# Kernel optimization log

Measured on AMD Instinct MI355X. Metric: run time of the kernel, lower is better.

The kernel has to match this reference:

```python
import jax, jax.numpy as jnp
import numpy as np
from jax.scipy.linalg import expm


def setup_inputs() -> dict:
    key = jax.random.key(0)
    k1, k2, k3 = jax.random.split(key, 3)
    B, T, d = 64, 4096, 16
    Z = jax.random.normal(k1, (B, T, 2), dtype=jnp.float32)
    A1 = jax.random.normal(k2, (d, d), dtype=jnp.float32)
    A2 = jax.random.normal(k3, (d, d), dtype=jnp.float32)
    return {"Z": Z, "A1": A1, "A2": A2}


def reference(Z, A1, A2):
    # Z: [B, T, 2]; A1, A2: [d, d] learned params
    d = A1.shape[0]
    S1 = A1 - A1.T  # skew-symmetric
    S2 = A2 - A2.T
    # per-timestep increment matrices: expm(z1*S1 + z2*S2), shape [B, T, d, d]
    G = Z[..., 0, None, None] * S1 + Z[..., 1, None, None] * S2
    M = expm(G)
    # X_0 = I; X_t = X_{t-1} @ M[:, t] for t = 1..T-1  (M[:, 0] is unused,
    # exactly as in the original loop starting at t=1).
    matmul = lambda a, b: jnp.einsum('...ij,...jk->...ik', a, b)
    prefix = jax.lax.associative_scan(matmul, M[:, 1:], axis=1)  # [B, T-1, d, d]
    eye = jnp.broadcast_to(jnp.eye(d, dtype=Z.dtype), (Z.shape[0], 1, d, d))
    A = jnp.concatenate([eye, prefix], axis=1)  # [B, T, d, d]
    B_inv = jnp.linalg.inv(A)
    return (A, B_inv)
```

## Files before the change

### kernel.cpp

```cpp
#include <hip/hip_runtime.h>

#define NB 64
#define NT 4096
#define CH 8
#define KC (NT/CH)
#define GPB 16
#define NA 128
#define NM 14
#define PI_F 3.14159265358979f

#define C3c (1.f/6.f)
#define C4c (1.f/24.f)
#define C5c (1.f/120.f)
#define C6c (1.f/720.f)
#define C7c (1.f/5040.f)
#define C8c (1.f/40320.f)

template<int K>
__device__ __forceinline__ void mm_step(float acc[16], const float a[16], const float b[16]) {
  float bb[16];
#pragma unroll
  for (int e = 0; e < 16; ++e)
    bb[e] = __int_as_float(__builtin_amdgcn_ds_swizzle(__float_as_int(b[e]), (K << 7) | 0x13));
#pragma unroll
  for (int rr = 0; rr < 4; ++rr) {
    const float a0 = __int_as_float(__builtin_amdgcn_mov_dpp(__float_as_int(a[rr*4+0]), K*0x55, 0xF, 0xF, true));
    const float a1 = __int_as_float(__builtin_amdgcn_mov_dpp(__float_as_int(a[rr*4+1]), K*0x55, 0xF, 0xF, true));
    const float a2 = __int_as_float(__builtin_amdgcn_mov_dpp(__float_as_int(a[rr*4+2]), K*0x55, 0xF, 0xF, true));
    const float a3 = __int_as_float(__builtin_amdgcn_mov_dpp(__float_as_int(a[rr*4+3]), K*0x55, 0xF, 0xF, true));
#pragma unroll
    for (int cc = 0; cc < 4; ++cc)
      acc[rr*4+cc] = fmaf(a3, bb[12+cc], fmaf(a2, bb[8+cc], fmaf(a1, bb[4+cc], fmaf(a0, bb[cc], acc[rr*4+cc]))));
  }
}
__device__ __forceinline__ void mmreg(float acc[16], const float a[16], const float b[16]) {
  mm_step<0>(acc, a, b); mm_step<1>(acc, a, b);
  mm_step<2>(acc, a, b); mm_step<3>(acc, a, b);
}

__global__ __launch_bounds__(256) void k0_prep(const float* __restrict__ A1,
                                               const float* __restrict__ A2,
                                               float* __restrict__ ws) {
  __shared__ float S[2][256], W2[4][256], W3[8][256], W4[16][256];
  const int tid = threadIdx.x;
  {
    int i_ = tid >> 4, j_ = tid & 15;
    S[0][tid] = A1[i_*16+j_] - A1[j_*16+i_];
    S[1][tid] = A2[i_*16+j_] - A2[j_*16+i_];
  }
  __syncthreads();
  const int i = tid >> 4, j = tid & 15;
#pragma unroll
  for (int p = 0; p < 4; ++p) {
    const float* a = S[p>>1]; const float* bm = S[p&1];
    float acc = 0.f;
    for (int k = 0; k < 16; ++k) acc = fmaf(a[i*16+k], bm[k*16+j], acc);
    W2[p][tid] = acc;
  }
  __syncthreads();
#pragma unroll
  for (int p = 0; p < 8; ++p) {
    const float* a = S[p>>2]; const float* bm = W2[p&3];
    float acc = 0.f;
    for (int k = 0; k < 16; ++k) acc = fmaf(a[i*16+k], bm[k*16+j], acc);
    W3[p][tid] = acc;
  }
  __syncthreads();
#pragma unroll
  for (int p = 0; p < 16; ++p) {
    const float* a = S[p>>3]; const float* bm = W3[p&7];
    float acc = 0.f;
    for (int k = 0; k < 16; ++k) acc = fmaf(a[i*16+k], bm[k*16+j], acc);
    W4[p][tid] = acc;
  }
  __syncthreads();
  float* M = ws + NA;
  M[ 0*256+tid] = S[0][tid];
  M[ 1*256+tid] = S[1][tid];
  M[ 2*256+tid] = W2[0][tid];
  M[ 3*256+tid] = W2[1][tid] + W2[2][tid];
  M[ 4*256+tid] = W2[3][tid];
  M[ 5*256+tid] = W3[0][tid];
  M[ 6*256+tid] = W3[1][tid] + W3[2][tid] + W3[4][tid];
  M[ 7*256+tid] = W3[3][tid] + W3[5][tid] + W3[6][tid];
  M[ 8*256+tid] = W3[7][tid];
  M[ 9*256+tid] = W4[0][tid];
  M[10*256+tid] = W4[1][tid] + W4[2][tid] + W4[4][tid] + W4[8][tid];
  M[11*256+tid] = W4[3][tid] + W4[5][tid] + W4[6][tid] + W4[9][tid] + W4[10][tid] + W4[12][tid];
  M[12*256+tid] = W4[7][tid] + W4[11][tid] + W4[13][tid] + W4[14][tid];
  M[13*256+tid] = W4[15][tid];
  if (tid < NA) {
    const float th = (float)tid * (PI_F / NA);
    const float c = cosf(th), s = sinf(th);
    float v[16];
    float n2 = 0.f;
#pragma unroll
    for (int jj = 0; jj < 16; ++jj) { v[jj] = sinf(1.7f*(float)(jj+1) + th) + 0.25f; n2 += v[jj]*v[jj]; }
    float inv = rsqrtf(n2);
#pragma unroll
    for (int jj = 0; jj < 16; ++jj) v[jj] *= inv;
    float lam = 0.f;
    for (int it = 0; it < 14; ++it) {
      float w[16];
#pragma unroll
      for (int ii = 0; ii < 16; ++ii) {
        float a1 = 0.f, a2 = 0.f;
#pragma unroll
        for (int jj = 0; jj < 16; ++jj) { a1 = fmaf(S[0][ii*16+jj], v[jj], a1); a2 = fmaf(S[1][ii*16+jj], v[jj], a2); }
        w[ii] = c*a1 + s*a2;
      }
      n2 = 0.f;
#pragma unroll
      for (int ii = 0; ii < 16; ++ii) n2 += w[ii]*w[ii];
      lam = sqrtf(n2);
      inv = (lam > 1e-20f) ? 1.f/lam : 0.f;
#pragma unroll
      for (int ii = 0; ii < 16; ++ii) v[ii] = w[ii]*inv;
    }
    ws[tid] = lam * 1.05f;
  }
}

__global__ __launch_bounds__(256, 2) void k1_chunk(const float* __restrict__ Z,
                                                   const float* __restrict__ wsrc,
                                                   float* __restrict__ Aout)
{
  __shared__ float Qs[NM*256];
  __shared__ float rhos[NA];
  const int tid = threadIdx.x;
  for (int e = tid; e < NM*256; e += 256) Qs[e] = wsrc[NA + e];
  if (tid < NA) rhos[tid] = wsrc[tid];
  __syncthreads();

  const int g  = tid >> 4;
  const int u  = tid & 15;
  const int tr = u >> 2;
  const int tc = u & 3;
  const int gw = (tid & 63) >> 4;
  const int qbase = (4*tr)*16 + 4*tc;

  const int cid    = blockIdx.x * GPB + g;
  const int b      = cid >> 9;
  const int kchunk = cid & (KC-1);
  const int t0     = kchunk * CH;

  const float trtc = (tr == tc) ? 1.f : 0.f;
  const int tz = t0 + u;
  float2 za = *(const float2*)&Z[(size_t)(b*NT + (tz < NT ? tz : NT-1)) * 2];

  float lt[16];
#pragma unroll
  for (int rr = 0; rr < 4; ++rr)
#pragma unroll
    for (int cc = 0; cc < 4; ++cc) lt[rr*4+cc] = (rr == cc) ? trtc : 0.f;

  const int fstep = (kchunk == 0) ? 1 : 0;

  for (int tt = 0; tt < CH; ++tt) {
    const size_t obase = (size_t)(b*NT + t0 + tt) * 256 + (size_t)(tr*64) + 4*tc;

    const int src = (gw << 4) + tt;
    float z1 = __shfl(za.x, src);
    float z2 = __shfl(za.y, src);
    float r_ = sqrtf(z1*z1 + z2*z2);
    float th = atan2f(z2, z1);
    if (th < 0.f) th += PI_F;
    int idx = ((int)(th * ((float)NA / PI_F) + 0.5f)) & (NA - 1);
    float nrm = r_ * rhos[idx];
    nrm = fmaxf(nrm, __shfl_xor(nrm, 16));
    nrm = fmaxf(nrm, __shfl_xor(nrm, 32));
    int s = 0;
    if (nrm > 1.0f) s = (int)ceilf(log2f(nrm));
    const float scl = exp2f(-(float)s);

    if (kchunk == 0 && tt == 0) {
#pragma unroll
      for (int rr = 0; rr < 4; ++rr)
        *(float4*)&Aout[obase + rr*16] =
          make_float4(lt[rr*4+0], lt[rr*4+1], lt[rr*4+2], lt[rr*4+3]);
      continue;
    }

    const float x = z1*scl, y = z2*scl;
    const float x2 = x*x, xy = x*y, y2 = y*y;
    const float x3 = x2*x, x2y = x2*y, xy2 = x*y2, y3 = y2*y;
    const float zc[NM] = { x, y, x2, xy, y2, x3, x2y, xy2, y3,
                           x2*x2, x3*y, x2*y2, x*y3, y2*y2 };
    const float WP[NM] = { 1.f,1.f, .5f,.5f,.5f, C3c,C3c,C3c,C3c, 0.f,0.f,0.f,0.f,0.f };
    const float WU[NM] = { C5c,C5c, C6c,C6c,C6c, C7c,C7c,C7c,C7c, C8c,C8c,C8c,C8c,C8c };

    float pp[16], uu[16], g4[16];
#pragma unroll
    for (int rr = 0; rr < 4; ++rr)
#pragma unroll
      for (int cc = 0; cc < 4; ++cc) {
        pp[rr*4+cc] = (rr == cc) ? trtc : 0.f;
        uu[rr*4+cc] = (rr == cc) ? trtc * C4c : 0.f;
        g4[rr*4+cc] = 0.f;
      }
#pragma unroll
    for (int m = 0; m < NM; ++m) {
      const float am = zc[m] * WP[m];
      const float bm = zc[m] * WU[m];
#pragma unroll
      for (int rr = 0; rr < 4; ++rr) {
        float4 v = *(const float4*)&Qs[m*256 + rr*16 + qbase];
        if (m < 9) {
          pp[rr*4+0] = fmaf(am, v.x, pp[rr*4+0]);
          pp[rr*4+1] = fmaf(am, v.y, pp[rr*4+1]);
          pp[rr*4+2] = fmaf(am, v.z, pp[rr*4+2]);
          pp[rr*4+3] = fmaf(am, v.w, pp[rr*4+3]);
        } else {
          g4[rr*4+0] = fmaf(zc[m], v.x, g4[rr*4+0]);
          g4[rr*4+1] = fmaf(zc[m], v.y, g4[rr*4+1]);
          g4[rr*4+2] = fmaf(zc[m], v.z, g4[rr*4+2]);
          g4[rr*4+3] = fmaf(zc[m], v.w, g4[rr*4+3]);
        }
        uu[rr*4+0] = fmaf(bm, v.x, uu[rr*4+0]);
        uu[rr*4+1] = fmaf(bm, v.y, uu[rr*4+1]);
        uu[rr*4+2] = fmaf(bm, v.z, uu[rr*4+2]);
        uu[rr*4+3] = fmaf(bm, v.w, uu[rr*4+3]);
      }
    }

    mmreg(pp, g4, uu);

    for (int q = 0; q < s; ++q) {
      float acc[16];
#pragma unroll
      for (int e = 0; e < 16; ++e) acc[e] = 0.f;
      mmreg(acc, pp, pp);
#pragma unroll
      for (int e = 0; e < 16; ++e) pp[e] = acc[e];
    }
    if (tt == fstep) {
#pragma unroll
      for (int e = 0; e < 16; ++e) lt[e] = pp[e];
    } else {
      float acc[16];
#pragma unroll
      for (int e = 0; e < 16; ++e) acc[e] = 0.f;
      mmreg(acc, lt, pp);
#pragma unroll
      for (int e = 0; e < 16; ++e) lt[e] = acc[e];
    }
#pragma unroll
    for (int rr = 0; rr < 4; ++rr)
      *(float4*)&Aout[obase + rr*16] =
        make_float4(lt[rr*4+0], lt[rr*4+1], lt[rr*4+2], lt[rr*4+3]);
  }
}

#define ROWB 72
#define MATS (4*ROWB)
#define LGS (2*MATS + 8)
#define BX 0
#define BY MATS
#define WSYNC() asm volatile("s_waitcnt lgkmcnt(0)" ::: "memory")

#define MM_FMA(A_, B0_, B1_, B2_, B3_, base) \
  acc[base+0] = fmaf(A_.w, B3_.x, fmaf(A_.z, B2_.x, fmaf(A_.y, B1_.x, fmaf(A_.x, B0_.x, acc[base+0])))); \
  acc[base+1] = fmaf(A_.w, B3_.y, fmaf(A_.z, B2_.y, fmaf(A_.y, B1_.y, fmaf(A_.x, B0_.y, acc[base+1])))); \
  acc[base+2] = fmaf(A_.w, B3_.z, fmaf(A_.z, B2_.z, fmaf(A_.y, B1_.z, fmaf(A_.x, B0_.z, acc[base+2])))); \
  acc[base+3] = fmaf(A_.w, B3_.w, fmaf(A_.z, B2_.w, fmaf(A_.y, B1_.w, fmaf(A_.x, B0_.w, acc[base+3]))));

template<bool CLR>
__device__ __forceinline__ void mmg(float acc[16], const float* sb, int offA, int offB,
                                    const int xA[4], const int xB[4], int trR) {
  if (CLR) {
#pragma unroll
    for (int e = 0; e < 16; ++e) acc[e] = 0.f;
  }
#pragma unroll
  for (int kk = 0; kk < 4; ++kk) {
    const float* pa = sb + offA + trR + xA[kk];
    const float* pb = sb + offB + kk*ROWB + xB[kk];
    float4 a0 = *(const float4*)(pa +  0);
    float4 a1 = *(const float4*)(pa + 16);
    float4 a2 = *(const float4*)(pa + 32);
    float4 a3 = *(const float4*)(pa + 48);
    float4 b0 = *(const float4*)(pb +  0);
    float4 b1 = *(const float4*)(pb + 16);
    float4 b2 = *(const float4*)(pb + 32);
    float4 b3 = *(const float4*)(pb + 48);
    MM_FMA(a0, b0, b1, b2, b3, 0)
    MM_FMA(a1, b0, b1, b2, b3, 4)
    MM_FMA(a2, b0, b1, b2, b3, 8)
    MM_FMA(a3, b0, b1, b2, b3, 12)
  }
}

__device__ __forceinline__ void st4(float* sb, int offD, const float v[16], int trR, int xD) {
  float* p = sb + offD + trR + xD;
#pragma unroll
  for (int rr = 0; rr < 4; ++rr)
    *(float4*)(p + rr*16) = make_float4(v[rr*4+0], v[rr*4+1], v[rr*4+2], v[rr*4+3]);
}

__global__ __launch_bounds__(256) void k2a(const float* __restrict__ Aout,
                                           float* __restrict__ Binv) {
  __shared__ float Cy[256], Lt[256];
  const int tid = threadIdx.x, i = tid >> 4, j = tid & 15;
  const int b = blockIdx.x >> 5, sb = blockIdx.x & 31;
  Cy[tid] = (i == j) ? 1.f : 0.f;
  float nxt = Aout[((size_t)(b*NT + (sb*16)*CH + CH - 1))*256 + tid];
  __syncthreads();
  for (int q = 0; q < 16; ++q) {
    const int k = sb*16 + q;
    Binv[((size_t)(b*NT + k*CH))*256 + tid] = Cy[tid];
    Lt[tid] = nxt;
    __syncthreads();
    if (q < 15) nxt = Aout[((size_t)(b*NT + (k+1)*CH + CH - 1))*256 + tid];
    float a2 = 0.f;
#pragma unroll
    for (int m = 0; m < 16; ++m) a2 = fmaf(Cy[i*16+m], Lt[m*16+j], a2);
    __syncthreads();
    Cy[tid] = a2;
    __syncthreads();
  }
  Binv[((size_t)(b*NT + sb*128 + 1))*256 + tid] = Cy[tid];
}

__global__ __launch_bounds__(256) void k2b(float* __restrict__ Binv) {
  __shared__ float Cy[256], Lt[256];
  const int tid = threadIdx.x, i = tid >> 4, j = tid & 15;
  const int b = blockIdx.x;
  Cy[tid] = (i == j) ? 1.f : 0.f;
  float nxt = Binv[((size_t)(b*NT + 1))*256 + tid];
  __syncthreads();
  for (int sb2 = 0; sb2 < 32; ++sb2) {
    Binv[((size_t)(b*NT + sb2*128 + 2))*256 + tid] = Cy[tid];
    Lt[tid] = nxt;
    __syncthreads();
    if (sb2 < 31) nxt = Binv[((size_t)(b*NT + (sb2+1)*128 + 1))*256 + tid];
    float a2 = 0.f;
#pragma unroll
    for (int m = 0; m < 16; ++m) a2 = fmaf(Cy[i*16+m], Lt[m*16+j], a2);
    __syncthreads();
    Cy[tid] = a2;
    __syncthreads();
  }
}

__global__ __launch_bounds__(256, 2) void k3_apply(float* __restrict__ Aout,
                                                   float* __restrict__ Binv)
{
  __shared__ __align__(16) float lds[GPB * LGS];
  __shared__ float SupL[256];
  const int tid = threadIdx.x;
  const int g   = tid >> 4;
  const int u   = tid & 15;
  const int tr  = u >> 2;
  const int tc  = u & 3;
  const int trR = tr * ROWB;
  float* sb_ = lds + g * LGS;
  const int xA[4] = { ((0^tr)<<2), ((1^tr)<<2), ((2^tr)<<2), ((3^tr)<<2) };
  const int xB[4] = { ((tc^0)<<2), ((tc^1)<<2), ((tc^2)<<2), ((tc^3)<<2) };
  const int xD    = ((tc^tr)<<2);

  const int b   = blockIdx.x >> 5;
  const int sbq = blockIdx.x & 31;
  const int k   = sbq*16 + g;
  const int t0  = k * CH;

  SupL[tid] = Binv[((size_t)(b*NT + sbq*128 + 2))*256 + tid];
  {
    const float* srcp = &Binv[((size_t)(b*NT + k*CH))*256];
#pragma unroll
    for (int rr = 0; rr < 4; ++rr) {
      float4 v = *(const float4*)&srcp[rr*64 + 4*u];
      *(float4*)&sb_[BX + rr*ROWB + tr*16 + ((tc^rr)<<2)] = v;
    }
  }
  __syncthreads();

  float wt[16];
  {
    float* acc = wt;
#pragma unroll
    for (int e = 0; e < 16; ++e) acc[e] = 0.f;
#pragma unroll
    for (int kk = 0; kk < 4; ++kk) {
      const float* pb = sb_ + BX + kk*ROWB + xB[kk];
      float4 b0 = *(const float4*)(pb +  0);
      float4 b1 = *(const float4*)(pb + 16);
      float4 b2 = *(const float4*)(pb + 32);
      float4 b3 = *(const float4*)(pb + 48);
      float4 a0 = *(const float4*)&SupL[(4*tr+0)*16 + 4*kk];
      float4 a1 = *(const float4*)&SupL[(4*tr+1)*16 + 4*kk];
      float4 a2 = *(const float4*)&SupL[(4*tr+2)*16 + 4*kk];
      float4 a3 = *(const float4*)&SupL[(4*tr+3)*16 + 4*kk];
      MM_FMA(a0, b0, b1, b2, b3, 0)
      MM_FMA(a1, b0, b1, b2, b3, 4)
      MM_FMA(a2, b0, b1, b2, b3, 8)
      MM_FMA(a3, b0, b1, b2, b3, 12)
    }
  }
  st4(sb_, BY, wt, trR, xD);
  WSYNC();

  float acc[16];
  for (int tt = 0; tt < CH; ++tt) {
    const size_t base = ((size_t)(b*NT + t0 + tt))*256;
#pragma unroll
    for (int rr = 0; rr < 4; ++rr) {
      float4 v = *(const float4*)&Aout[base + rr*64 + 4*u];
      *(float4*)&sb_[BX + rr*ROWB + tr*16 + ((tc^rr)<<2)] = v;
    }
    WSYNC();
    mmg<true>(acc, sb_, BY, BX, xA, xB, trR);
    const size_t obase = base + (size_t)(tr*64) + 4*tc;
#pragma unroll
    for (int rr = 0; rr < 4; ++rr)
      *(float4*)&Aout[obase + rr*16] =
        make_float4(acc[rr*4+0], acc[rr*4+1], acc[rr*4+2], acc[rr*4+3]);
    st4(sb_, BX, acc, trR, xD); WSYNC();
    const float* pt = sb_ + BX + tc*ROWB + ((tr^tc)<<2);
    float4 f0 = *(const float4*)(pt +  0);
    float4 f1 = *(const float4*)(pt + 16);
    float4 f2 = *(const float4*)(pt + 32);
    float4 f3 = *(const float4*)(pt + 48);
    *(float4*)&Binv[obase +  0] = make_float4(f0.x, f1.x, f2.x, f3.x);
    *(float4*)&Binv[obase + 16] = make_float4(f0.y, f1.y, f2.y, f3.y);
    *(float4*)&Binv[obase + 32] = make_float4(f0.z, f1.z, f2.z, f3.z);
    *(float4*)&Binv[obase + 48] = make_float4(f0.w, f1.w, f2.w, f3.w);
    WSYNC();
  }
}

extern "C" void kernel_launch(void* const* d_in, const int* in_sizes, int n_in,
                              void* d_out, int out_size, void* d_ws, size_t ws_size,
                              hipStream_t stream) {
  const float* Z  = (const float*)d_in[0];
  const float* A1 = (const float*)d_in[1];
  const float* A2 = (const float*)d_in[2];
  float* ws   = (float*)d_ws;
  float* Aout = (float*)d_out;
  float* Binv = Aout + (size_t)NB * NT * 256;

  k0_prep<<<1, 256, 0, stream>>>(A1, A2, ws);
  k1_chunk<<<NB * KC / GPB, 256, 0, stream>>>(Z, ws, Aout);
  k2a<<<NB * 32, 256, 0, stream>>>(Aout, Binv);
  k2b<<<NB, 256, 0, stream>>>(Binv);
  k3_apply<<<NB * 32, 256, 0, stream>>>(Aout, Binv);
}
```

Measured before the change: 542.5 us.

## Replace serial carry scans with parallel Hillis-Steele scans and register-tiled apply

```diff
diff --git a/kernel.cpp b/kernel.cpp
--- a/kernel.cpp
+++ b/kernel.cpp
@@ -8,6 +8,7 @@
 #define NA 128
 #define NM 14
 #define PI_F 3.14159265358979f
+#define XPAD 20
 
 #define C3c (1.f/6.f)
 #define C4c (1.f/24.f)
@@ -36,6 +37,20 @@
 __device__ __forceinline__ void mmreg(float acc[16], const float a[16], const float b[16]) {
   mm_step<0>(acc, a, b); mm_step<1>(acc, a, b);
   mm_step<2>(acc, a, b); mm_step<3>(acc, a, b);
+}
+
+__device__ __forceinline__ void ld_tile(float p[16], const float* base, int tr, int tc) {
+#pragma unroll
+  for (int rr = 0; rr < 4; ++rr) {
+    float4 v = *(const float4*)&base[(4*tr+rr)*16 + 4*tc];
+    p[rr*4+0]=v.x; p[rr*4+1]=v.y; p[rr*4+2]=v.z; p[rr*4+3]=v.w;
+  }
+}
+__device__ __forceinline__ void st_tile(float* base, const float p[16], int tr, int tc) {
+#pragma unroll
+  for (int rr = 0; rr < 4; ++rr)
+    *(float4*)&base[(4*tr+rr)*16 + 4*tc] =
+      make_float4(p[rr*4+0], p[rr*4+1], p[rr*4+2], p[rr*4+3]);
 }
 
 __global__ __launch_bounds__(256) void k0_prep(const float* __restrict__ A1,
@@ -251,180 +266,142 @@
   }
 }
 
-#define ROWB 72
-#define MATS (4*ROWB)
-#define LGS (2*MATS + 8)
-#define BX 0
-#define BY MATS
-#define WSYNC() asm volatile("s_waitcnt lgkmcnt(0)" ::: "memory")
-
-#define MM_FMA(A_, B0_, B1_, B2_, B3_, base) \
-  acc[base+0] = fmaf(A_.w, B3_.x, fmaf(A_.z, B2_.x, fmaf(A_.y, B1_.x, fmaf(A_.x, B0_.x, acc[base+0])))); \
-  acc[base+1] = fmaf(A_.w, B3_.y, fmaf(A_.z, B2_.y, fmaf(A_.y, B1_.y, fmaf(A_.x, B0_.y, acc[base+1])))); \
-  acc[base+2] = fmaf(A_.w, B3_.z, fmaf(A_.z, B2_.z, fmaf(A_.y, B1_.z, fmaf(A_.x, B0_.z, acc[base+2])))); \
-  acc[base+3] = fmaf(A_.w, B3_.w, fmaf(A_.z, B2_.w, fmaf(A_.y, B1_.w, fmaf(A_.x, B0_.w, acc[base+3]))));
-
-template<bool CLR>
-__device__ __forceinline__ void mmg(float acc[16], const float* sb, int offA, int offB,
-                                    const int xA[4], const int xB[4], int trR) {
-  if (CLR) {
-#pragma unroll
-    for (int e = 0; e < 16; ++e) acc[e] = 0.f;
-  }
-#pragma unroll
-  for (int kk = 0; kk < 4; ++kk) {
-    const float* pa = sb + offA + trR + xA[kk];
-    const float* pb = sb + offB + kk*ROWB + xB[kk];
-    float4 a0 = *(const float4*)(pa +  0);
-    float4 a1 = *(const float4*)(pa + 16);
-    float4 a2 = *(const float4*)(pa + 32);
-    float4 a3 = *(const float4*)(pa + 48);
-    float4 b0 = *(const float4*)(pb +  0);
-    float4 b1 = *(const float4*)(pb + 16);
-    float4 b2 = *(const float4*)(pb + 32);
-    float4 b3 = *(const float4*)(pb + 48);
-    MM_FMA(a0, b0, b1, b2, b3, 0)
-    MM_FMA(a1, b0, b1, b2, b3, 4)
-    MM_FMA(a2, b0, b1, b2, b3, 8)
-    MM_FMA(a3, b0, b1, b2, b3, 12)
-  }
-}
-
-__device__ __forceinline__ void st4(float* sb, int offD, const float v[16], int trR, int xD) {
-  float* p = sb + offD + trR + xD;
-#pragma unroll
-  for (int rr = 0; rr < 4; ++rr)
-    *(float4*)(p + rr*16) = make_float4(v[rr*4+0], v[rr*4+1], v[rr*4+2], v[rr*4+3]);
-}
 
 __global__ __launch_bounds__(256) void k2a(const float* __restrict__ Aout,
                                            float* __restrict__ Binv) {
-  __shared__ float Cy[256], Lt[256];
-  const int tid = threadIdx.x, i = tid >> 4, j = tid & 15;
+  __shared__ float xch[16*16*XPAD];
+  const int tid = threadIdx.x;
+  const int g = tid >> 4, u = tid & 15, tr = u >> 2, tc = u & 3;
   const int b = blockIdx.x >> 5, sb = blockIdx.x & 31;
-  Cy[tid] = (i == j) ? 1.f : 0.f;
-  float nxt = Aout[((size_t)(b*NT + (sb*16)*CH + CH - 1))*256 + tid];
-  __syncthreads();
-  for (int q = 0; q < 16; ++q) {
-    const int k = sb*16 + q;
-    Binv[((size_t)(b*NT + k*CH))*256 + tid] = Cy[tid];
-    Lt[tid] = nxt;
+  const int k = sb*16 + g;
+
+  float p[16];
+  ld_tile(p, &Aout[((size_t)(b*NT + k*CH + CH-1))*256], tr, tc);
+
+#pragma unroll
+  for (int r = 1; r < 16; r <<= 1) {
+    float* mine = &xch[(g*16+u)*XPAD];
+#pragma unroll
+    for (int rr = 0; rr < 4; ++rr)
+      *(float4*)&mine[4*rr] = make_float4(p[rr*4+0], p[rr*4+1], p[rr*4+2], p[rr*4+3]);
     __syncthreads();
-    if (q < 15) nxt = Aout[((size_t)(b*NT + (k+1)*CH + CH - 1))*256 + tid];
-    float a2 = 0.f;
-#pragma unroll
-    for (int m = 0; m < 16; ++m) a2 = fmaf(Cy[i*16+m], Lt[m*16+j], a2);
+    if (g >= r) {
+      const float* nb = &xch[((g-r)*16+u)*XPAD];
+      float a[16];
+#pragma unroll
+      for (int rr = 0; rr < 4; ++rr) {
+        float4 v = *(const float4*)&nb[4*rr];
+        a[rr*4+0]=v.x; a[rr*4+1]=v.y; a[rr*4+2]=v.z; a[rr*4+3]=v.w;
+      }
+      float acc[16];
+#pragma unroll
+      for (int e = 0; e < 16; ++e) acc[e] = 0.f;
+      mmreg(acc, a, p);
+#pragma unroll
+      for (int e = 0; e < 16; ++e) p[e] = acc[e];
+    }
     __syncthreads();
-    Cy[tid] = a2;
+  }
+
+  const float trtc = (tr == tc) ? 1.f : 0.f;
+  if (g == 0) {
+    float idt[16];
+#pragma unroll
+    for (int rr = 0; rr < 4; ++rr)
+#pragma unroll
+      for (int cc = 0; cc < 4; ++cc) idt[rr*4+cc] = (rr == cc) ? trtc : 0.f;
+    st_tile(&Binv[((size_t)(b*NT + k*CH))*256], idt, tr, tc);
+  }
+  if (g < 15)
+    st_tile(&Binv[((size_t)(b*NT + (k+1)*CH))*256], p, tr, tc);
+  else
+    st_tile(&Binv[((size_t)(b*NT + 128*sb + 1))*256], p, tr, tc);
+}
+
+__global__ __launch_bounds__(512) void k2b(float* __restrict__ Binv) {
+  __shared__ float xch[32*16*XPAD];
+  const int tid = threadIdx.x;
+  const int g = tid >> 4, u = tid & 15, tr = u >> 2, tc = u & 3;
+  const int b = blockIdx.x;
+
+  float p[16];
+  ld_tile(p, &Binv[((size_t)(b*NT + 128*g + 1))*256], tr, tc);
+
+#pragma unroll
+  for (int r = 1; r < 32; r <<= 1) {
+    float* mine = &xch[(g*16+u)*XPAD];
+#pragma unroll
+    for (int rr = 0; rr < 4; ++rr)
+      *(float4*)&mine[4*rr] = make_float4(p[rr*4+0], p[rr*4+1], p[rr*4+2], p[rr*4+3]);
     __syncthreads();
-  }
-  Binv[((size_t)(b*NT + sb*128 + 1))*256 + tid] = Cy[tid];
-}
-
-__global__ __launch_bounds__(256) void k2b(float* __restrict__ Binv) {
-  __shared__ float Cy[256], Lt[256];
-  const int tid = threadIdx.x, i = tid >> 4, j = tid & 15;
-  const int b = blockIdx.x;
-  Cy[tid] = (i == j) ? 1.f : 0.f;
-  float nxt = Binv[((size_t)(b*NT + 1))*256 + tid];
-  __syncthreads();
-  for (int sb2 = 0; sb2 < 32; ++sb2) {
-    Binv[((size_t)(b*NT + sb2*128 + 2))*256 + tid] = Cy[tid];
-    Lt[tid] = nxt;
+    if (g >= r) {
+      const float* nb = &xch[((g-r)*16+u)*XPAD];
+      float a[16];
+#pragma unroll
+      for (int rr = 0; rr < 4; ++rr) {
+        float4 v = *(const float4*)&nb[4*rr];
+        a[rr*4+0]=v.x; a[rr*4+1]=v.y; a[rr*4+2]=v.z; a[rr*4+3]=v.w;
+      }
+      float acc[16];
+#pragma unroll
+      for (int e = 0; e < 16; ++e) acc[e] = 0.f;
+      mmreg(acc, a, p);
+#pragma unroll
+      for (int e = 0; e < 16; ++e) p[e] = acc[e];
+    }
     __syncthreads();
-    if (sb2 < 31) nxt = Binv[((size_t)(b*NT + (sb2+1)*128 + 1))*256 + tid];
-    float a2 = 0.f;
-#pragma unroll
-    for (int m = 0; m < 16; ++m) a2 = fmaf(Cy[i*16+m], Lt[m*16+j], a2);
-    __syncthreads();
-    Cy[tid] = a2;
-    __syncthreads();
-  }
+  }
+
+  const float trtc = (tr == tc) ? 1.f : 0.f;
+  if (g == 0) {
+    float idt[16];
+#pragma unroll
+    for (int rr = 0; rr < 4; ++rr)
+#pragma unroll
+      for (int cc = 0; cc < 4; ++cc) idt[rr*4+cc] = (rr == cc) ? trtc : 0.f;
+    st_tile(&Binv[((size_t)(b*NT + 2))*256], idt, tr, tc);
+  }
+  if (g < 31)
+    st_tile(&Binv[((size_t)(b*NT + 128*(g+1) + 2))*256], p, tr, tc);
 }
 
 __global__ __launch_bounds__(256, 2) void k3_apply(float* __restrict__ Aout,
                                                    float* __restrict__ Binv)
 {
-  __shared__ __align__(16) float lds[GPB * LGS];
-  __shared__ float SupL[256];
   const int tid = threadIdx.x;
-  const int g   = tid >> 4;
-  const int u   = tid & 15;
-  const int tr  = u >> 2;
-  const int tc  = u & 3;
-  const int trR = tr * ROWB;
-  float* sb_ = lds + g * LGS;
-  const int xA[4] = { ((0^tr)<<2), ((1^tr)<<2), ((2^tr)<<2), ((3^tr)<<2) };
-  const int xB[4] = { ((tc^0)<<2), ((tc^1)<<2), ((tc^2)<<2), ((tc^3)<<2) };
-  const int xD    = ((tc^tr)<<2);
-
-  const int b   = blockIdx.x >> 5;
-  const int sbq = blockIdx.x & 31;
-  const int k   = sbq*16 + g;
-  const int t0  = k * CH;
-
-  SupL[tid] = Binv[((size_t)(b*NT + sbq*128 + 2))*256 + tid];
-  {
-    const float* srcp = &Binv[((size_t)(b*NT + k*CH))*256];
-#pragma unroll
-    for (int rr = 0; rr < 4; ++rr) {
-      float4 v = *(const float4*)&srcp[rr*64 + 4*u];
-      *(float4*)&sb_[BX + rr*ROWB + tr*16 + ((tc^rr)<<2)] = v;
-    }
-  }
-  __syncthreads();
-
-  float wt[16];
-  {
-    float* acc = wt;
-#pragma unroll
-    for (int e = 0; e < 16; ++e) acc[e] = 0.f;
-#pragma unroll
-    for (int kk = 0; kk < 4; ++kk) {
-      const float* pb = sb_ + BX + kk*ROWB + xB[kk];
-      float4 b0 = *(const float4*)(pb +  0);
-      float4 b1 = *(const float4*)(pb + 16);
-      float4 b2 = *(const float4*)(pb + 32);
-      float4 b3 = *(const float4*)(pb + 48);
-      float4 a0 = *(const float4*)&SupL[(4*tr+0)*16 + 4*kk];
-      float4 a1 = *(const float4*)&SupL[(4*tr+1)*16 + 4*kk];
-      float4 a2 = *(const float4*)&SupL[(4*tr+2)*16 + 4*kk];
-      float4 a3 = *(const float4*)&SupL[(4*tr+3)*16 + 4*kk];
-      MM_FMA(a0, b0, b1, b2, b3, 0)
-      MM_FMA(a1, b0, b1, b2, b3, 4)
-      MM_FMA(a2, b0, b1, b2, b3, 8)
-      MM_FMA(a3, b0, b1, b2, b3, 12)
-    }
-  }
-  st4(sb_, BY, wt, trR, xD);
-  WSYNC();
-
-  float acc[16];
+  const int g = tid >> 4, u = tid & 15, tr = u >> 2, tc = u & 3;
+  const int gw = (tid & 63) >> 4;
+  const int b = blockIdx.x >> 5, sb = blockIdx.x & 31;
+  const int k = sb*16 + g;
+  const int t0 = k * CH;
+
+  float su[16], ek[16], w[16];
+  ld_tile(su, &Binv[((size_t)(b*NT + 128*sb + 2))*256], tr, tc);
+  ld_tile(ek, &Binv[((size_t)(b*NT + k*CH))*256], tr, tc);
+#pragma unroll
+  for (int e = 0; e < 16; ++e) w[e] = 0.f;
+  mmreg(w, su, ek);
+  __syncthreads();
+
+  const int bidx = (gw*16 + tc*4 + tr) * 4;
+
+#pragma unroll
   for (int tt = 0; tt < CH; ++tt) {
     const size_t base = ((size_t)(b*NT + t0 + tt))*256;
-#pragma unroll
-    for (int rr = 0; rr < 4; ++rr) {
-      float4 v = *(const float4*)&Aout[base + rr*64 + 4*u];
-      *(float4*)&sb_[BX + rr*ROWB + tr*16 + ((tc^rr)<<2)] = v;
-    }
-    WSYNC();
-    mmg<true>(acc, sb_, BY, BX, xA, xB, trR);
-    const size_t obase = base + (size_t)(tr*64) + 4*tc;
-#pragma unroll
-    for (int rr = 0; rr < 4; ++rr)
-      *(float4*)&Aout[obase + rr*16] =
-        make_float4(acc[rr*4+0], acc[rr*4+1], acc[rr*4+2], acc[rr*4+3]);
-    st4(sb_, BX, acc, trR, xD); WSYNC();
-    const float* pt = sb_ + BX + tc*ROWB + ((tr^tc)<<2);
-    float4 f0 = *(const float4*)(pt +  0);
-    float4 f1 = *(const float4*)(pt + 16);
-    float4 f2 = *(const float4*)(pt + 32);
-    float4 f3 = *(const float4*)(pt + 48);
-    *(float4*)&Binv[obase +  0] = make_float4(f0.x, f1.x, f2.x, f3.x);
-    *(float4*)&Binv[obase + 16] = make_float4(f0.y, f1.y, f2.y, f3.y);
-    *(float4*)&Binv[obase + 32] = make_float4(f0.z, f1.z, f2.z, f3.z);
-    *(float4*)&Binv[obase + 48] = make_float4(f0.w, f1.w, f2.w, f3.w);
-    WSYNC();
+    float lt[16], acc[16], tp[16];
+    ld_tile(lt, &Aout[base], tr, tc);
+#pragma unroll
+    for (int e = 0; e < 16; ++e) acc[e] = 0.f;
+    mmreg(acc, w, lt);
+    st_tile(&Aout[base], acc, tr, tc);
+#pragma unroll
+    for (int e = 0; e < 16; ++e)
+      tp[e] = __int_as_float(__builtin_amdgcn_ds_bpermute(bidx, __float_as_int(acc[e])));
+    float* dst = &Binv[base];
+#pragma unroll
+    for (int rr = 0; rr < 4; ++rr)
+      *(float4*)&dst[(4*tr+rr)*16 + 4*tc] =
+        make_float4(tp[rr], tp[4+rr], tp[8+rr], tp[12+rr]);
   }
 }
 
@@ -441,6 +418,6 @@
   k0_prep<<<1, 256, 0, stream>>>(A1, A2, ws);
   k1_chunk<<<NB * KC / GPB, 256, 0, stream>>>(Z, ws, Aout);
   k2a<<<NB * 32, 256, 0, stream>>>(Aout, Binv);
-  k2b<<<NB, 256, 0, stream>>>(Binv);
+  k2b<<<NB, 512, 0, stream>>>(Binv);
   k3_apply<<<NB * 32, 256, 0, stream>>>(Aout, Binv);
 }
```

After: 562.6 us. 3.7% more time.
